# Kernel tuning notes

Measured on AMD Instinct MI355X. Metric: run time of the kernel, lower is better.

## Reference

```python
import jax, jax.numpy as jnp
import numpy as np

N = 50000          # nodes
E = 800000         # edges (avg degree 16)
IN, HID, OUT = 128, 128, 32
BN_EPS = 1e-5


def gcn_conv(x, W, b, src, dst):
    """PyG GCNConv: D^-1/2 (A+I) D^-1/2 (x @ W) + b, self-loops included."""
    h = x @ W                                                  # [N, out]
    ones = jnp.ones((src.shape[0],), dtype=x.dtype)
    deg = jax.ops.segment_sum(ones, dst, num_segments=N) + 1.0  # in-degree + self-loop
    dis = jax.lax.rsqrt(deg)                                    # deg^-1/2
    norm = dis[src] * dis[dst]                                  # [E]
    msg = h[src] * norm[:, None]                                # gather + scale, [E, out]
    agg = jax.ops.segment_sum(msg, dst, num_segments=N)         # scatter-add
    agg = agg + h * (dis * dis)[:, None]                        # self-loop term (norm = 1/deg_i)
    return agg + b


def bn_relu(h, g, be):
    # BatchNorm1d in training mode: batch statistics over the node dimension
    mu = jnp.mean(h, axis=0)
    var = jnp.mean((h - mu) ** 2, axis=0)  # biased variance, as torch BN
    return jax.nn.relu((h - mu) * jax.lax.rsqrt(var + BN_EPS) * g + be)


def setup_inputs() -> dict:
    key = jax.random.key(0)
    ks = jax.random.split(key, 8)
    x = jax.random.normal(ks[0], (N, IN), dtype=jnp.float32)
    edge_index = jax.random.randint(ks[1], (2, E), 0, N, dtype=jnp.int64)
    W0 = jax.random.normal(ks[2], (IN, HID), dtype=jnp.float32) / np.sqrt(IN)
    W1 = jax.random.normal(ks[3], (HID, HID), dtype=jnp.float32) / np.sqrt(HID)
    W2 = jax.random.normal(ks[4], (HID, OUT), dtype=jnp.float32) / np.sqrt(HID)
    return {
        "x": x, "edge_index": edge_index,
        "W0": W0, "b0": jnp.zeros((HID,), jnp.float32),
        "g0": jnp.ones((HID,), jnp.float32), "be0": jnp.zeros((HID,), jnp.float32),
        "W1": W1, "b1": jnp.zeros((HID,), jnp.float32),
        "g1": jnp.ones((HID,), jnp.float32), "be1": jnp.zeros((HID,), jnp.float32),
        "W2": W2, "b2": jnp.zeros((OUT,), jnp.float32),
    }


def reference(x, edge_index, W0, b0, g0, be0, W1, b1, g1, be1, W2, b2):
    src, dst = edge_index[0], edge_index[1]
    # block 0: conv -> BN -> ReLU -> (dropout: eval, identity) -> residual
    h = bn_relu(gcn_conv(x, W0, b0, src, dst), g0, be0)
    x = h + x  # use_residual, in_channels == hidden, res_proj is None
    # block 1
    h = bn_relu(gcn_conv(x, W1, b1, src, dst), g1, be1)
    x = h + x
    # final conv + log_softmax over classes
    out = gcn_conv(x, W2, b2, src, dst)
    return jax.nn.log_softmax(out, axis=1)
```

## Files before the change

kernel.cpp:

```cpp
#include <hip/hip_runtime.h>
#include <math.h>

#define NN 50000
#define NNP (NN + 1)
#define NE 800000
#define NEP 1150000
#define NBLK 49

typedef __attribute__((ext_vector_type(8))) short short8;
typedef __attribute__((ext_vector_type(4))) float float4v;

__device__ inline unsigned int f2bf(float f) {
  unsigned int u = __float_as_uint(f);
  return (u + 0x7fffu + ((u >> 16) & 1u)) >> 16;
}
__device__ inline unsigned int pack2bf(float lo, float hi) {
  return f2bf(lo) | (f2bf(hi) << 16);
}
__device__ inline float bflo(unsigned int p) { return __uint_as_float(p << 16); }
__device__ inline float bfhi(unsigned int p) { return __uint_as_float(p & 0xffff0000u); }

__device__ inline void bn_fold(const float* __restrict__ gstat, const float* __restrict__ g,
                               const float* __restrict__ be, float* __restrict__ bnabS, int tid) {
  if (tid < 128) {
    float s = 0.f, q = 0.f;
    #pragma unroll
    for (int r = 0; r < 8; r++) {
      s += gstat[r * 256 + tid];
      q += gstat[r * 256 + 128 + tid];
    }
    const float inv = 1.f / (float)NN;
    float m = s * inv;
    float var = q * inv - m * m;
    float a = rsqrtf(var + 1e-5f) * g[tid];
    bnabS[tid] = a;
    bnabS[128 + tid] = be[tid] - m * a;
  }
}


__global__ __launch_bounds__(256) void k_init(int* __restrict__ deg8, float* __restrict__ gstat,
                                              int* __restrict__ csr,
                                              const float* __restrict__ W0, const float* __restrict__ W1,
                                              const float* __restrict__ W2,
                                              unsigned short* __restrict__ wt16) {
  int i = blockIdx.x * 256 + threadIdx.x;
  if (i < NEP) csr[i] = NN;
  if (i < 8 * NN) deg8[i] = 0;
  if (i < 4096) gstat[i] = 0.f;
  if (i < 32768) {
    int w = i >> 14;
    int rem = i & 16383;
    int k = rem >> 7;
    int n = rem & 127;
    const float* W = w ? W1 : W0;
    wt16[w * 16384 + n * 128 + k] = (unsigned short)f2bf(W[k * 128 + n]);
  } else if (i < 36864) {
    int idx = i - 32768;
    int n = idx >> 7;
    int k = idx & 127;
    wt16[32768 + n * 128 + k] = (unsigned short)f2bf(W2[k * 32 + n]);
  }
}


__global__ __launch_bounds__(256) void k_cnt(const int* __restrict__ dst, int* __restrict__ deg8) {
  int e = blockIdx.x * 256 + threadIdx.x;
  if (e < NE) atomicAdd(&deg8[(e & 7) * NN + dst[e]], 1);
}


__global__ __launch_bounds__(1024) void k_scan1(const int* __restrict__ deg8, int* __restrict__ degtot,
                                                int* __restrict__ excl, int* __restrict__ blksum) {
  __shared__ int smW[16];
  int t = threadIdx.x;
  int i = blockIdx.x * 1024 + t;
  int wv = t >> 6, ln = t & 63;
  int tot = 0;
  if (i < NN) {
    #pragma unroll
    for (int j = 0; j < 8; j++) tot += deg8[j * NN + i];
    degtot[i] = tot;
  }
  int v = (i < NN) ? ((tot + 7) & ~7) : 0;
  int sc = v;
  #pragma unroll
  for (int off = 1; off < 64; off <<= 1) {
    int u = __shfl_up(sc, off);
    if (ln >= off) sc += u;
  }
  if (ln == 63) smW[wv] = sc;
  __syncthreads();
  if (t < 64) {
    int wsum = (t < 16) ? smW[t] : 0;
    int s2 = wsum;
    #pragma unroll
    for (int off = 1; off < 16; off <<= 1) {
      int u = __shfl_up(s2, off);
      if (t >= off) s2 += u;
    }
    if (t < 16) smW[t] = s2 - wsum;
    if (t == 15) blksum[blockIdx.x] = s2;
  }
  __syncthreads();
  if (i < NN) excl[i] = (sc - v) + smW[wv];
}


__global__ __launch_bounds__(256) void k_scan3(int* __restrict__ rowstart, const int* __restrict__ blksum,
                                               const int* __restrict__ degtot, int* __restrict__ cursor,
                                               float* __restrict__ dis,
                                               unsigned short* __restrict__ hs16, float* __restrict__ h2) {
  __shared__ int offS;
  int tid = threadIdx.x;
  int i = blockIdx.x * 256 + tid;
  int myblk = blockIdx.x >> 2;
  if (tid < 64) {
    int bv = (tid < NBLK) ? blksum[tid] : 0;
    int sc = bv;
    #pragma unroll
    for (int off = 1; off < 64; off <<= 1) {
      int u = __shfl_up(sc, off);
      if (tid >= off) sc += u;
    }
    int pre = (myblk > 0) ? __shfl(sc, myblk - 1) : 0;
    int total = __shfl(sc, NBLK - 1);
    if (tid == 0) {
      offS = pre;
      if (blockIdx.x == 0) rowstart[NN] = total;
    }
  }
  __syncthreads();
  int boff = offS;
  if (i < NN) {
    int rs = rowstart[i] + boff;
    rowstart[i] = rs;
    cursor[i] = rs;
    dis[i] = rsqrtf((float)degtot[i] + 1.0f);
  }
  if (i < 64) {
    int slice = i >> 5, c = i & 31;
    ((unsigned int*)(hs16 + (size_t)slice * ((size_t)NNP * 64) + (size_t)NN * 64))[c] = 0u;
  }
  if (i < 32) h2[(size_t)NN * 32 + i] = 0.f;
}


__global__ __launch_bounds__(256) void k_fill(const int* __restrict__ src, const int* __restrict__ dst,
                                              int* __restrict__ cursor, int* __restrict__ csr_src) {
  int e = blockIdx.x * 256 + threadIdx.x;
  if (e >= NE) return;
  int d = dst[e];
  int p = atomicAdd(&cursor[d], 1);
  csr_src[p] = src[e];
}


__global__ __launch_bounds__(256) void k_gemm128(const float* __restrict__ X,
                                                 const unsigned short* __restrict__ Wt,
                                                 const float* __restrict__ dis,
                                                 unsigned short* __restrict__ hs16, int M) {
  __shared__ char smem[52224];
  unsigned short* A  = (unsigned short*)smem;
  unsigned short* Bt = (unsigned short*)(smem + 17408);
  float* C = (float*)smem;
  const int tid = threadIdx.x;
  const int row0 = blockIdx.x * 64;

  {
    int c4 = tid & 31;
    #pragma unroll
    for (int i = 0; i < 8; i++) {
      int r = (tid >> 5) + i * 8;
      int gr = row0 + r;
      float4 v = make_float4(0.f, 0.f, 0.f, 0.f);
      if (gr < M) v = *(const float4*)(X + (size_t)gr * 128 + c4 * 4);
      *(uint2*)(A + r * 136 + c4 * 4) = make_uint2(pack2bf(v.x, v.y), pack2bf(v.z, v.w));
    }
  }
  {
    int r = tid >> 1, h = (tid & 1) * 64;
    const uint4* src = (const uint4*)(Wt + r * 128 + h);
    uint4* dst = (uint4*)(Bt + r * 136 + h);
    #pragma unroll
    for (int i = 0; i < 8; i++) dst[i] = src[i];
  }
  __syncthreads();

  const int wv = tid >> 6;
  const int l = tid & 63;
  const int lm = l & 15;
  const int lq = l >> 4;

  float4v acc[8];
  #pragma unroll
  for (int j = 0; j < 8; j++) acc[j] = (float4v)(0.f);

  const unsigned short* Arow = A + (wv * 16 + lm) * 136 + lq * 8;
  #pragma unroll
  for (int ks = 0; ks < 4; ks++) {
    short8 af = *(const short8*)(Arow + ks * 32);
    #pragma unroll
    for (int j = 0; j < 8; j++) {
      short8 bf = *(const short8*)(Bt + (j * 16 + lm) * 136 + lq * 8 + ks * 32);
      acc[j] = __builtin_amdgcn_mfma_f32_16x16x32_bf16(af, bf, acc[j], 0, 0, 0);
    }
  }
  __syncthreads();

  #pragma unroll
  for (int j = 0; j < 8; j++) {
    int col = j * 16 + lm;
    int rbase = wv * 16 + lq * 4;
    #pragma unroll
    for (int r = 0; r < 4; r++) C[(rbase + r) * 132 + col] = acc[j][r];
  }
  __syncthreads();

  {
    #pragma unroll
    for (int i = 0; i < 4; i++) {
      int idx = tid + i * 256;
      int slice = idx >> 9;
      int r = (idx >> 3) & 63;
      int ch = idx & 7;
      int gr = row0 + r;
      if (gr < M) {
        float d = dis[gr];
        const float* cp = C + r * 132 + slice * 64 + ch * 8;
        uint4 u;
        u.x = pack2bf(cp[0] * d, cp[1] * d);
        u.y = pack2bf(cp[2] * d, cp[3] * d);
        u.z = pack2bf(cp[4] * d, cp[5] * d);
        u.w = pack2bf(cp[6] * d, cp[7] * d);
        *(uint4*)(hs16 + (size_t)slice * ((size_t)NNP * 64) + (size_t)gr * 64 + ch * 8) = u;
      }
    }
  }
}


__global__ __launch_bounds__(256) void k_gemm128f(const unsigned short* __restrict__ O16,
                                                  const float* __restrict__ Xin,
                                                  unsigned short* __restrict__ XA16,
                                                  const float* __restrict__ gstat,
                                                  const float* __restrict__ g,
                                                  const float* __restrict__ be,
                                                  const unsigned short* __restrict__ Wt,
                                                  const float* __restrict__ dis,
                                                  unsigned short* __restrict__ hs16, int M) {
  __shared__ char smem[52224];
  __shared__ float bnabS[256];
  unsigned short* A  = (unsigned short*)smem;
  unsigned short* Bt = (unsigned short*)(smem + 17408);
  float* C = (float*)smem;
  const int tid = threadIdx.x;
  const int row0 = blockIdx.x * 64;

  bn_fold(gstat, g, be, bnabS, tid);
  __syncthreads();

  {
    int c = tid & 15;
    float4 alo = *(const float4*)(bnabS + c * 8);
    float4 ahi = *(const float4*)(bnabS + c * 8 + 4);
    float4 clo = *(const float4*)(bnabS + 128 + c * 8);
    float4 chi = *(const float4*)(bnabS + 128 + c * 8 + 4);
    #pragma unroll
    for (int i = 0; i < 4; i++) {
      int r = (tid >> 4) + i * 16;
      int gr = row0 + r;
      uint4 u = make_uint4(0u, 0u, 0u, 0u);
      if (gr < M) {
        uint4 ou = *(const uint4*)(O16 + (size_t)gr * 128 + c * 8);
        float4 xlo = *(const float4*)(Xin + (size_t)gr * 128 + c * 8);
        float4 xhi = *(const float4*)(Xin + (size_t)gr * 128 + c * 8 + 4);
        float v0 = fmaxf(bflo(ou.x) * alo.x + clo.x, 0.f) + xlo.x;
        float v1 = fmaxf(bfhi(ou.x) * alo.y + clo.y, 0.f) + xlo.y;
        float v2 = fmaxf(bflo(ou.y) * alo.z + clo.z, 0.f) + xlo.z;
        float v3 = fmaxf(bfhi(ou.y) * alo.w + clo.w, 0.f) + xlo.w;
        float v4 = fmaxf(bflo(ou.z) * ahi.x + chi.x, 0.f) + xhi.x;
        float v5 = fmaxf(bfhi(ou.z) * ahi.y + chi.y, 0.f) + xhi.y;
        float v6 = fmaxf(bflo(ou.w) * ahi.z + chi.z, 0.f) + xhi.z;
        float v7 = fmaxf(bfhi(ou.w) * ahi.w + chi.w, 0.f) + xhi.w;
        u.x = pack2bf(v0, v1);
        u.y = pack2bf(v2, v3);
        u.z = pack2bf(v4, v5);
        u.w = pack2bf(v6, v7);
        *(uint4*)(XA16 + (size_t)gr * 128 + c * 8) = u;
      }
      *(uint4*)(A + r * 136 + c * 8) = u;
    }
  }
  {
    int r = tid >> 1, h = (tid & 1) * 64;
    const uint4* src = (const uint4*)(Wt + r * 128 + h);
    uint4* dst = (uint4*)(Bt + r * 136 + h);
    #pragma unroll
    for (int i = 0; i < 8; i++) dst[i] = src[i];
  }
  __syncthreads();

  const int wv = tid >> 6;
  const int l = tid & 63;
  const int lm = l & 15;
  const int lq = l >> 4;

  float4v acc[8];
  #pragma unroll
  for (int j = 0; j < 8; j++) acc[j] = (float4v)(0.f);

  const unsigned short* Arow = A + (wv * 16 + lm) * 136 + lq * 8;
  #pragma unroll
  for (int ks = 0; ks < 4; ks++) {
    short8 af = *(const short8*)(Arow + ks * 32);
    #pragma unroll
    for (int j = 0; j < 8; j++) {
      short8 bf = *(const short8*)(Bt + (j * 16 + lm) * 136 + lq * 8 + ks * 32);
      acc[j] = __builtin_amdgcn_mfma_f32_16x16x32_bf16(af, bf, acc[j], 0, 0, 0);
    }
  }
  __syncthreads();

  #pragma unroll
  for (int j = 0; j < 8; j++) {
    int col = j * 16 + lm;
    int rbase = wv * 16 + lq * 4;
    #pragma unroll
    for (int r = 0; r < 4; r++) C[(rbase + r) * 132 + col] = acc[j][r];
  }
  __syncthreads();

  {
    #pragma unroll
    for (int i = 0; i < 4; i++) {
      int idx = tid + i * 256;
      int slice = idx >> 9;
      int r = (idx >> 3) & 63;
      int ch = idx & 7;
      int gr = row0 + r;
      if (gr < M) {
        float d = dis[gr];
        const float* cp = C + r * 132 + slice * 64 + ch * 8;
        uint4 u;
        u.x = pack2bf(cp[0] * d, cp[1] * d);
        u.y = pack2bf(cp[2] * d, cp[3] * d);
        u.z = pack2bf(cp[4] * d, cp[5] * d);
        u.w = pack2bf(cp[6] * d, cp[7] * d);
        *(uint4*)(hs16 + (size_t)slice * ((size_t)NNP * 64) + (size_t)gr * 64 + ch * 8) = u;
      }
    }
  }
}


__global__ __launch_bounds__(256) void k_gemm32mf(const unsigned short* __restrict__ O16,
                                                  const unsigned short* __restrict__ XA16,
                                                  const float* __restrict__ gstat,
                                                  const float* __restrict__ g,
                                                  const float* __restrict__ be,
                                                  const unsigned short* __restrict__ Wt2,
                                                  const float* __restrict__ dis,
                                                  float* __restrict__ H, int M) {
  __shared__ char smem[26112];
  __shared__ float bnabS[256];
  unsigned short* A   = (unsigned short*)smem;
  unsigned short* Bt2 = (unsigned short*)(smem + 17408);
  float* C = (float*)smem;
  const int tid = threadIdx.x;
  const int row0 = blockIdx.x * 64;

  bn_fold(gstat, g, be, bnabS, tid);
  __syncthreads();

  {
    int c = tid & 15;
    float4 alo = *(const float4*)(bnabS + c * 8);
    float4 ahi = *(const float4*)(bnabS + c * 8 + 4);
    float4 clo = *(const float4*)(bnabS + 128 + c * 8);
    float4 chi = *(const float4*)(bnabS + 128 + c * 8 + 4);
    #pragma unroll
    for (int i = 0; i < 4; i++) {
      int r = (tid >> 4) + i * 16;
      int gr = row0 + r;
      uint4 u = make_uint4(0u, 0u, 0u, 0u);
      if (gr < M) {
        uint4 ou = *(const uint4*)(O16 + (size_t)gr * 128 + c * 8);
        uint4 xu = *(const uint4*)(XA16 + (size_t)gr * 128 + c * 8);
        float v0 = fmaxf(bflo(ou.x) * alo.x + clo.x, 0.f) + bflo(xu.x);
        float v1 = fmaxf(bfhi(ou.x) * alo.y + clo.y, 0.f) + bfhi(xu.x);
        float v2 = fmaxf(bflo(ou.y) * alo.z + clo.z, 0.f) + bflo(xu.y);
        float v3 = fmaxf(bfhi(ou.y) * alo.w + clo.w, 0.f) + bfhi(xu.y);
        float v4 = fmaxf(bflo(ou.z) * ahi.x + chi.x, 0.f) + bflo(xu.z);
        float v5 = fmaxf(bfhi(ou.z) * ahi.y + chi.y, 0.f) + bfhi(xu.z);
        float v6 = fmaxf(bflo(ou.w) * ahi.z + chi.z, 0.f) + bflo(xu.w);
        float v7 = fmaxf(bfhi(ou.w) * ahi.w + chi.w, 0.f) + bfhi(xu.w);
        u.x = pack2bf(v0, v1);
        u.y = pack2bf(v2, v3);
        u.z = pack2bf(v4, v5);
        u.w = pack2bf(v6, v7);
      }
      *(uint4*)(A + r * 136 + c * 8) = u;
    }
  }
  {
    int r = tid >> 3, h = (tid & 7) * 16;
    const uint4* src = (const uint4*)(Wt2 + r * 128 + h);
    uint4* dst = (uint4*)(Bt2 + r * 136 + h);
    dst[0] = src[0];
    dst[1] = src[1];
  }
  __syncthreads();

  const int wv = tid >> 6;
  const int l = tid & 63;
  const int lm = l & 15;
  const int lq = l >> 4;

  float4v acc[2];
  acc[0] = (float4v)(0.f);
  acc[1] = (float4v)(0.f);

  const unsigned short* Arow = A + (wv * 16 + lm) * 136 + lq * 8;
  #pragma unroll
  for (int ks = 0; ks < 4; ks++) {
    short8 af = *(const short8*)(Arow + ks * 32);
    #pragma unroll
    for (int j = 0; j < 2; j++) {
      short8 bf = *(const short8*)(Bt2 + (j * 16 + lm) * 136 + lq * 8 + ks * 32);
      acc[j] = __builtin_amdgcn_mfma_f32_16x16x32_bf16(af, bf, acc[j], 0, 0, 0);
    }
  }
  __syncthreads();

  #pragma unroll
  for (int j = 0; j < 2; j++) {
    int col = j * 16 + lm;
    int rbase = wv * 16 + lq * 4;
    #pragma unroll
    for (int r = 0; r < 4; r++) C[(rbase + r) * 36 + col] = acc[j][r];
  }
  __syncthreads();

  {
    #pragma unroll
    for (int i = 0; i < 2; i++) {
      int idx = tid + i * 256;
      int r = idx >> 3;
      int ch = idx & 7;
      int gr = row0 + r;
      if (gr < M) {
        float d = dis[gr];
        const float* cp = C + r * 36 + ch * 4;
        float4 v = make_float4(cp[0] * d, cp[1] * d, cp[2] * d, cp[3] * d);
        *(float4*)(H + (size_t)gr * 32 + ch * 4) = v;
      }
    }
  }
}


__global__ __launch_bounds__(256) void k_agg128s(const unsigned short* __restrict__ Hs,
                                                 const float* __restrict__ dis,
                                                 const int* __restrict__ rowstart,
                                                 const int* __restrict__ csr_src,
                                                 const float* __restrict__ bias,
                                                 unsigned short* __restrict__ out16,
                                                 float* __restrict__ gstat) {
  __shared__ float smS[4][128], smQ[4][128];
  const int tid = threadIdx.x;
  const int wv = tid >> 6;
  const int lane = tid & 63;
  const int node_sub = lane >> 3;
  const int fl = lane & 7;
  const int base = node_sub * 8;
  const int w = blockIdx.x * 32 + wv * 8 + node_sub;
  const bool act = w < NN;
  const unsigned short* __restrict__ S0 = Hs + fl * 8;
  const unsigned short* __restrict__ S1 = Hs + (size_t)NNP * 64 + fl * 8;
  float di = act ? dis[w] : 0.f;
  int e0 = 0, e1 = 0;
  if (act) { e0 = rowstart[w]; e1 = rowstart[w + 1]; }

  float a0[8], a1[8];
  #pragma unroll
  for (int j = 0; j < 8; j++) { a0[j] = 0.f; a1[j] = 0.f; }

  int idxCur = (e0 < e1) ? csr_src[e0 + fl] : 0;
  for (int e = e0; e < e1; e += 8) {
    int cur = idxCur;
    if (e + 8 < e1) idxCur = csr_src[e + 8 + fl];
    int s0 = __shfl(cur, base + 0), s1 = __shfl(cur, base + 1);
    int s2 = __shfl(cur, base + 2), s3 = __shfl(cur, base + 3);
    int s4 = __shfl(cur, base + 4), s5 = __shfl(cur, base + 5);
    int s6 = __shfl(cur, base + 6), s7 = __shfl(cur, base + 7);
    uint4 g0 = *(const uint4*)(S0 + (size_t)s0 * 64);
    uint4 g1 = *(const uint4*)(S0 + (size_t)s1 * 64);
    uint4 g2 = *(const uint4*)(S0 + (size_t)s2 * 64);
    uint4 g3 = *(const uint4*)(S0 + (size_t)s3 * 64);
    uint4 g4 = *(const uint4*)(S0 + (size_t)s4 * 64);
    uint4 g5 = *(const uint4*)(S0 + (size_t)s5 * 64);
    uint4 g6 = *(const uint4*)(S0 + (size_t)s6 * 64);
    uint4 g7 = *(const uint4*)(S0 + (size_t)s7 * 64);
    uint4 h0 = *(const uint4*)(S1 + (size_t)s0 * 64);
    uint4 h1 = *(const uint4*)(S1 + (size_t)s1 * 64);
    uint4 h2 = *(const uint4*)(S1 + (size_t)s2 * 64);
    uint4 h3 = *(const uint4*)(S1 + (size_t)s3 * 64);
    uint4 h4 = *(const uint4*)(S1 + (size_t)s4 * 64);
    uint4 h5 = *(const uint4*)(S1 + (size_t)s5 * 64);
    uint4 h6 = *(const uint4*)(S1 + (size_t)s6 * 64);
    uint4 h7 = *(const uint4*)(S1 + (size_t)s7 * 64);
    a0[0] += ((bflo(g0.x) + bflo(g1.x)) + (bflo(g2.x) + bflo(g3.x))) + ((bflo(g4.x) + bflo(g5.x)) + (bflo(g6.x) + bflo(g7.x)));
    a0[1] += ((bfhi(g0.x) + bfhi(g1.x)) + (bfhi(g2.x) + bfhi(g3.x))) + ((bfhi(g4.x) + bfhi(g5.x)) + (bfhi(g6.x) + bfhi(g7.x)));
    a0[2] += ((bflo(g0.y) + bflo(g1.y)) + (bflo(g2.y) + bflo(g3.y))) + ((bflo(g4.y) + bflo(g5.y)) + (bflo(g6.y) + bflo(g7.y)));
    a0[3] += ((bfhi(g0.y) + bfhi(g1.y)) + (bfhi(g2.y) + bfhi(g3.y))) + ((bfhi(g4.y) + bfhi(g5.y)) + (bfhi(g6.y) + bfhi(g7.y)));
    a0[4] += ((bflo(g0.z) + bflo(g1.z)) + (bflo(g2.z) + bflo(g3.z))) + ((bflo(g4.z) + bflo(g5.z)) + (bflo(g6.z) + bflo(g7.z)));
    a0[5] += ((bfhi(g0.z) + bfhi(g1.z)) + (bfhi(g2.z) + bfhi(g3.z))) + ((bfhi(g4.z) + bfhi(g5.z)) + (bfhi(g6.z) + bfhi(g7.z)));
    a0[6] += ((bflo(g0.w) + bflo(g1.w)) + (bflo(g2.w) + bflo(g3.w))) + ((bflo(g4.w) + bflo(g5.w)) + (bflo(g6.w) + bflo(g7.w)));
    a0[7] += ((bfhi(g0.w) + bfhi(g1.w)) + (bfhi(g2.w) + bfhi(g3.w))) + ((bfhi(g4.w) + bfhi(g5.w)) + (bfhi(g6.w) + bfhi(g7.w)));
    a1[0] += ((bflo(h0.x) + bflo(h1.x)) + (bflo(h2.x) + bflo(h3.x))) + ((bflo(h4.x) + bflo(h5.x)) + (bflo(h6.x) + bflo(h7.x)));
    a1[1] += ((bfhi(h0.x) + bfhi(h1.x)) + (bfhi(h2.x) + bfhi(h3.x))) + ((bfhi(h4.x) + bfhi(h5.x)) + (bfhi(h6.x) + bfhi(h7.x)));
    a1[2] += ((bflo(h0.y) + bflo(h1.y)) + (bflo(h2.y) + bflo(h3.y))) + ((bflo(h4.y) + bflo(h5.y)) + (bflo(h6.y) + bflo(h7.y)));
    a1[3] += ((bfhi(h0.y) + bfhi(h1.y)) + (bfhi(h2.y) + bfhi(h3.y))) + ((bfhi(h4.y) + bfhi(h5.y)) + (bfhi(h6.y) + bfhi(h7.y)));
    a1[4] += ((bflo(h0.z) + bflo(h1.z)) + (bflo(h2.z) + bflo(h3.z))) + ((bflo(h4.z) + bflo(h5.z)) + (bflo(h6.z) + bflo(h7.z)));
    a1[5] += ((bfhi(h0.z) + bfhi(h1.z)) + (bfhi(h2.z) + bfhi(h3.z))) + ((bfhi(h4.z) + bfhi(h5.z)) + (bfhi(h6.z) + bfhi(h7.z)));
    a1[6] += ((bflo(h0.w) + bflo(h1.w)) + (bflo(h2.w) + bflo(h3.w))) + ((bflo(h4.w) + bflo(h5.w)) + (bflo(h6.w) + bflo(h7.w)));
    a1[7] += ((bfhi(h0.w) + bfhi(h1.w)) + (bfhi(h2.w) + bfhi(h3.w))) + ((bfhi(h4.w) + bfhi(h5.w)) + (bfhi(h6.w) + bfhi(h7.w)));
  }

  float rv0[8], rv1[8];
  if (act) {
    uint4 sv0 = *(const uint4*)(S0 + (size_t)w * 64);
    uint4 sv1 = *(const uint4*)(S1 + (size_t)w * 64);
    float se0[8] = { bflo(sv0.x), bfhi(sv0.x), bflo(sv0.y), bfhi(sv0.y),
                     bflo(sv0.z), bfhi(sv0.z), bflo(sv0.w), bfhi(sv0.w) };
    float se1[8] = { bflo(sv1.x), bfhi(sv1.x), bflo(sv1.y), bfhi(sv1.y),
                     bflo(sv1.z), bfhi(sv1.z), bflo(sv1.w), bfhi(sv1.w) };
    #pragma unroll
    for (int j = 0; j < 8; j++) {
      rv0[j] = (a0[j] + se0[j]) * di + bias[fl * 8 + j];
      rv1[j] = (a1[j] + se1[j]) * di + bias[64 + fl * 8 + j];
    }
    uint4 u0, u1;
    u0.x = pack2bf(rv0[0], rv0[1]); u0.y = pack2bf(rv0[2], rv0[3]);
    u0.z = pack2bf(rv0[4], rv0[5]); u0.w = pack2bf(rv0[6], rv0[7]);
    u1.x = pack2bf(rv1[0], rv1[1]); u1.y = pack2bf(rv1[2], rv1[3]);
    u1.z = pack2bf(rv1[4], rv1[5]); u1.w = pack2bf(rv1[6], rv1[7]);
    *(uint4*)(out16 + (size_t)w * 128 + fl * 8)      = u0;
    *(uint4*)(out16 + (size_t)w * 128 + 64 + fl * 8) = u1;
  } else {
    #pragma unroll
    for (int j = 0; j < 8; j++) { rv0[j] = 0.f; rv1[j] = 0.f; }
  }

  float q0[8], q1[8];
  #pragma unroll
  for (int j = 0; j < 8; j++) { q0[j] = rv0[j] * rv0[j]; q1[j] = rv1[j] * rv1[j]; }
  #pragma unroll
  for (int off = 8; off <= 32; off <<= 1) {
    #pragma unroll
    for (int j = 0; j < 8; j++) {
      rv0[j] += __shfl_xor(rv0[j], off);
      q0[j]  += __shfl_xor(q0[j], off);
      rv1[j] += __shfl_xor(rv1[j], off);
      q1[j]  += __shfl_xor(q1[j], off);
    }
  }
  if (node_sub == 0) {
    #pragma unroll
    for (int j = 0; j < 8; j++) {
      smS[wv][fl * 8 + j] = rv0[j];      smQ[wv][fl * 8 + j] = q0[j];
      smS[wv][64 + fl * 8 + j] = rv1[j]; smQ[wv][64 + fl * 8 + j] = q1[j];
    }
  }
  __syncthreads();
  if (tid < 128) {
    float s = (smS[0][tid] + smS[1][tid]) + (smS[2][tid] + smS[3][tid]);
    float q = (smQ[0][tid] + smQ[1][tid]) + (smQ[2][tid] + smQ[3][tid]);
    int rep = blockIdx.x & 7;
    atomicAdd(&gstat[rep * 256 + tid], s);
    atomicAdd(&gstat[rep * 256 + 128 + tid], q);
  }
}


__global__ __launch_bounds__(256) void k_agg32lsm(const float* __restrict__ H2,
                                                  const float* __restrict__ dis,
                                                  const int* __restrict__ rowstart,
                                                  const int* __restrict__ csr_src,
                                                  const float* __restrict__ bias,
                                                  float* __restrict__ out) {
  int wave = (blockIdx.x * 256 + threadIdx.x) >> 6;
  int lane = threadIdx.x & 63;
  int half = lane >> 5;
  int l = lane & 31;
  int hbase = half * 32;
  int w = wave * 2 + half;
  if (w >= NN) return;
  const float* __restrict__ S = H2 + l;
  float di = dis[w];
  int e0 = rowstart[w], e1 = rowstart[w + 1];
  float acc = 0.f;
  for (int e = e0; e < e1; e += 8) {
    int myIdx = csr_src[e + (l & 7)];
    int s0 = __shfl(myIdx, hbase + 0), s1 = __shfl(myIdx, hbase + 1);
    int s2 = __shfl(myIdx, hbase + 2), s3 = __shfl(myIdx, hbase + 3);
    int s4 = __shfl(myIdx, hbase + 4), s5 = __shfl(myIdx, hbase + 5);
    int s6 = __shfl(myIdx, hbase + 6), s7 = __shfl(myIdx, hbase + 7);
    float h0 = S[(size_t)s0 * 32], h1 = S[(size_t)s1 * 32];
    float h2v = S[(size_t)s2 * 32], h3 = S[(size_t)s3 * 32];
    float h4 = S[(size_t)s4 * 32], h5 = S[(size_t)s5 * 32];
    float h6 = S[(size_t)s6 * 32], h7 = S[(size_t)s7 * 32];
    acc += ((h0 + h1) + (h2v + h3)) + ((h4 + h5) + (h6 + h7));
  }
  float v = (acc + S[(size_t)w * 32]) * di + bias[l];
  float m = v;
  #pragma unroll
  for (int off = 16; off >= 1; off >>= 1) m = fmaxf(m, __shfl_xor(m, off));
  float ex = expf(v - m);
  float s = ex;
  #pragma unroll
  for (int off = 16; off >= 1; off >>= 1) s += __shfl_xor(s, off);
  out[(size_t)w * 32 + l] = v - m - logf(s);
}


extern "C" void kernel_launch(void* const* d_in, const int* in_sizes, int n_in,
                              void* d_out, int out_size, void* d_ws, size_t ws_size,
                              hipStream_t stream) {
  const float* x   = (const float*)d_in[0];
  const int*   ei  = (const int*)d_in[1];
  const float* W0  = (const float*)d_in[2];
  const float* b0  = (const float*)d_in[3];
  const float* g0  = (const float*)d_in[4];
  const float* be0 = (const float*)d_in[5];
  const float* W1  = (const float*)d_in[6];
  const float* b1  = (const float*)d_in[7];
  const float* g1  = (const float*)d_in[8];
  const float* be1 = (const float*)d_in[9];
  const float* W2  = (const float*)d_in[10];
  const float* b2  = (const float*)d_in[11];
  float* out = (float*)d_out;
  const int* srcI = ei;
  const int* dstI = ei + NE;

  char* p = (char*)d_ws;
  auto take = [&](size_t bytes) { char* r = p; p += (bytes + 255) & ~(size_t)255; return (void*)r; };
  int*   deg8     = (int*)take((size_t)8 * NN * 4);
  int*   cursor   = (int*)take(NN * 4);
  int*   degtot   = (int*)take(NN * 4);
  int*   rowstart = (int*)take((NN + 1) * 4);
  int*   blksum   = (int*)take(64 * 4);
  float* dis      = (float*)take(NN * 4);
  int*   csr      = (int*)take((size_t)NEP * 4);
  float* gstat    = (float*)take(4096 * 4);
  unsigned short* wt16 = (unsigned short*)take((2 * 16384 + 4096) * 2);
  unsigned short* hs16 = (unsigned short*)take((size_t)NNP * 128 * 2);
  unsigned short* o16  = (unsigned short*)take((size_t)NN * 128 * 2);
  unsigned short* xA16 = (unsigned short*)take((size_t)NN * 128 * 2);
  float* h2       = (float*)take((size_t)NNP * 32 * 4);

  k_init<<<(NEP + 255) / 256, 256, 0, stream>>>(deg8, gstat, csr, W0, W1, W2, wt16);
  k_cnt<<<(NE + 255) / 256, 256, 0, stream>>>(dstI, deg8);
  k_scan1<<<NBLK, 1024, 0, stream>>>(deg8, degtot, rowstart, blksum);
  k_scan3<<<(NN + 255) / 256, 256, 0, stream>>>(rowstart, blksum, degtot, cursor, dis, hs16, h2);
  k_fill<<<(NE + 255) / 256, 256, 0, stream>>>(srcI, dstI, cursor, csr);

  const int aggGrid = (NN + 31) / 32;
  const int aggGrid32 = (NN + 7) / 8;

  k_gemm128<<<(NN + 63) / 64, 256, 0, stream>>>(x, wt16, dis, hs16, NN);
  k_agg128s<<<aggGrid, 256, 0, stream>>>(hs16, dis, rowstart, csr, b0, o16, gstat);

  k_gemm128f<<<(NN + 63) / 64, 256, 0, stream>>>(o16, x, xA16, gstat, g0, be0,
                                                 wt16 + 16384, dis, hs16, NN);
  k_agg128s<<<aggGrid, 256, 0, stream>>>(hs16, dis, rowstart, csr, b1, o16, gstat + 2048);

  k_gemm32mf<<<(NN + 63) / 64, 256, 0, stream>>>(o16, xA16, gstat + 2048, g1, be1,
                                                 wt16 + 32768, dis, h2, NN);
  k_agg32lsm<<<aggGrid32, 256, 0, stream>>>(h2, dis, rowstart, csr, b2, out);
}
```

Baseline: 303.5 us.

## Pre-bucket edges by destination range before CSR fill to localize atomics

The degree-count pass now also partitions edges into 7 buckets keyed by destination node range (dst>>13), writing (dst,src) pairs into per-bucket arrays via block-local then global atomic reservations. The CSR fill kernel then walks each bucket separately, so cursor atomics and csr writes from a group of blocks hit a narrower address range and should get better cache locality. This adds an extra 8-byte-per-edge write and read plus a bucket buffer in workspace. Bucket sizes depend on a uniform destination distribution staying under the fixed capacity.

```diff
diff --git a/kernel.cpp b/kernel.cpp
--- a/kernel.cpp
+++ b/kernel.cpp
@@ -6,6 +6,8 @@
 #define NE 800000
 #define NEP 1150000
 #define NBLK 49
+#define NBKT 7
+#define BCAP 262144
 
 typedef __attribute__((ext_vector_type(8))) short short8;
 typedef __attribute__((ext_vector_type(4))) float float4v;
@@ -40,7 +42,7 @@
 
 
 __global__ __launch_bounds__(256) void k_init(int* __restrict__ deg8, float* __restrict__ gstat,
-                                              int* __restrict__ csr,
+                                              int* __restrict__ csr, int* __restrict__ binCnt,
                                               const float* __restrict__ W0, const float* __restrict__ W1,
                                               const float* __restrict__ W2,
                                               unsigned short* __restrict__ wt16) {
@@ -48,6 +50,7 @@
   if (i < NEP) csr[i] = NN;
   if (i < 8 * NN) deg8[i] = 0;
   if (i < 4096) gstat[i] = 0.f;
+  if (i < NBKT) binCnt[i] = 0;
   if (i < 32768) {
     int w = i >> 14;
     int rem = i & 16383;
@@ -64,9 +67,26 @@
 }
 
 
-__global__ __launch_bounds__(256) void k_cnt(const int* __restrict__ dst, int* __restrict__ deg8) {
-  int e = blockIdx.x * 256 + threadIdx.x;
-  if (e < NE) atomicAdd(&deg8[(e & 7) * NN + dst[e]], 1);
+__global__ __launch_bounds__(1024) void k_binA(const int* __restrict__ src, const int* __restrict__ dst,
+                                               int* __restrict__ deg8, int* __restrict__ binCnt,
+                                               int2* __restrict__ bin) {
+  __shared__ int lcnt[NBKT], lbase[NBKT];
+  int tid = threadIdx.x;
+  if (tid < NBKT) lcnt[tid] = 0;
+  __syncthreads();
+  int e = blockIdx.x * 1024 + tid;
+  bool act = e < NE;
+  int d = 0, s = 0, b = 0, rank = 0;
+  if (act) {
+    d = dst[e]; s = src[e];
+    b = d >> 13;
+    atomicAdd(&deg8[(e & 7) * NN + d], 1);
+    rank = atomicAdd(&lcnt[b], 1);
+  }
+  __syncthreads();
+  if (tid < NBKT && lcnt[tid] > 0) lbase[tid] = atomicAdd(&binCnt[tid], lcnt[tid]);
+  __syncthreads();
+  if (act) bin[(size_t)b * BCAP + lbase[b] + rank] = make_int2(d, s);
 }
 
 
@@ -146,13 +166,18 @@
 }
 
 
-__global__ __launch_bounds__(256) void k_fill(const int* __restrict__ src, const int* __restrict__ dst,
-                                              int* __restrict__ cursor, int* __restrict__ csr_src) {
-  int e = blockIdx.x * 256 + threadIdx.x;
-  if (e >= NE) return;
-  int d = dst[e];
-  int p = atomicAdd(&cursor[d], 1);
-  csr_src[p] = src[e];
+__global__ __launch_bounds__(256) void k_fillB(const int2* __restrict__ bin, const int* __restrict__ binCnt,
+                                               int* __restrict__ cursor, int* __restrict__ csr_src) {
+  int b = blockIdx.x & 7;
+  if (b >= NBKT) return;
+  int q = blockIdx.x >> 3;
+  int cnt = binCnt[b];
+  const int2* __restrict__ B = bin + (size_t)b * BCAP;
+  for (int i = q * 256 + threadIdx.x; i < cnt; i += 64 * 256) {
+    int2 ds = B[i];
+    int p = atomicAdd(&cursor[ds.x], 1);
+    csr_src[p] = ds.y;
+  }
 }
 
 
@@ -651,8 +676,10 @@
   int*   degtot   = (int*)take(NN * 4);
   int*   rowstart = (int*)take((NN + 1) * 4);
   int*   blksum   = (int*)take(64 * 4);
+  int*   binCnt   = (int*)take(8 * 4);
   float* dis      = (float*)take(NN * 4);
   int*   csr      = (int*)take((size_t)NEP * 4);
+  int2*  bin      = (int2*)take((size_t)NBKT * BCAP * 8);
   float* gstat    = (float*)take(4096 * 4);
   unsigned short* wt16 = (unsigned short*)take((2 * 16384 + 4096) * 2);
   unsigned short* hs16 = (unsigned short*)take((size_t)NNP * 128 * 2);
@@ -660,11 +687,11 @@
   unsigned short* xA16 = (unsigned short*)take((size_t)NN * 128 * 2);
   float* h2       = (float*)take((size_t)NNP * 32 * 4);
 
-  k_init<<<(NEP + 255) / 256, 256, 0, stream>>>(deg8, gstat, csr, W0, W1, W2, wt16);
-  k_cnt<<<(NE + 255) / 256, 256, 0, stream>>>(dstI, deg8);
+  k_init<<<(NEP + 255) / 256, 256, 0, stream>>>(deg8, gstat, csr, binCnt, W0, W1, W2, wt16);
+  k_binA<<<(NE + 1023) / 1024, 1024, 0, stream>>>(srcI, dstI, deg8, binCnt, bin);
   k_scan1<<<NBLK, 1024, 0, stream>>>(deg8, degtot, rowstart, blksum);
   k_scan3<<<(NN + 255) / 256, 256, 0, stream>>>(rowstart, blksum, degtot, cursor, dis, hs16, h2);
-  k_fill<<<(NE + 255) / 256, 256, 0, stream>>>(srcI, dstI, cursor, csr);
+  k_fillB<<<512, 256, 0, stream>>>(bin, binCnt, cursor, csr);
 
   const int aggGrid = (NN + 31) / 32;
   const int aggGrid32 = (NN + 7) / 8;
```

Result: faster. 288.6 us (-4.9%).
